# Kernel optimization log

Hardware: AMD Instinct MI355X
Metric: run time of the kernel (lower is better)

The kernel has to match this reference:

```python
import jax, jax.numpy as jnp
import numpy as np

T, B, D = 20, 1024, 2312  # time_steps, batch, 2*34*34 (NMNIST flattened)


def setup_inputs() -> dict:
    key = jax.random.key(0)
    k1, k2, k3, k4 = jax.random.split(key, 4)
    return {
        "x": jax.random.normal(k1, (T, B, D), dtype=jnp.float32),
        # ATIC per-feature parameters (torch inits these to zero; small random
        # values used here so gradients/gating are non-trivial for kernel tests)
        "ac": jax.random.normal(k2, (D,), dtype=jnp.float32) * 0.1,
        "tw": jax.random.normal(k3, (D,), dtype=jnp.float32) * 0.1,
        "ig": jax.random.normal(k4, (D,), dtype=jnp.float32) * 0.1,
        # LIF scalar parameters (torch defaults)
        "membrane_decay": jnp.asarray(0.8, dtype=jnp.float32),
        "synaptic_decay": jnp.asarray(0.75, dtype=jnp.float32),
        "threshold": jnp.asarray(0.8, dtype=jnp.float32),
    }


def _atic(xt, ac, tw, ig):
    # AdaptiveTemporalInformationCompression.forward on one timestep [B, D]
    p = jax.nn.softmax(xt, axis=-1)
    entropy = -jnp.sum(p * jnp.log(p + 1e-8), axis=-1)          # [B]
    compression_mask = jax.nn.sigmoid(ac * entropy[:, None])    # [B, D]
    compressed = xt * compression_mask * jax.nn.sigmoid(tw) * jax.nn.sigmoid(ig)
    binding_strength = jnp.mean(jnp.abs(compressed))             # scalar
    return compressed * binding_strength


def reference(x, ac, tw, ig, membrane_decay, synaptic_decay, threshold):
    # Per-timestep ATIC gating feeding a LIF current/membrane recurrence with
    # sigmoid surrogate spikes (surrogate_alpha = 1.0) and soft reset.
    def step(carry, xt):
        i, v = carry
        i = synaptic_decay * i + _atic(xt, ac, tw, ig)
        v = membrane_decay * v + i
        s = jax.nn.sigmoid(v - threshold)  # surrogate spike
        v = v - s * threshold              # soft reset toward reset_potential=0
        return (i, v), s

    init = (jnp.zeros((B, D), x.dtype), jnp.zeros((B, D), x.dtype))
    _, spikes = jax.lax.scan(step, init, x)  # [T, B, D]
    return spikes
```

## Files before the change

kernel.cpp:

```cpp
#include <hip/hip_runtime.h>

#define T_STEPS 20
#define B_SIZE  1024
#define D_SIZE  2312
#define BD      (B_SIZE * D_SIZE)
#define BLOCK   256
#define ROW_F4  (D_SIZE / 4)
#define ROWS_PER_BLOCK 4

#define ACC_STRIDE 32
#define ENT_OFF    1024
#define GEFF_OFF   (ENT_OFF + T_STEPS * B_SIZE)
#define WS_WORDS   (GEFF_OFF + D_SIZE)

typedef float floatx4 __attribute__((ext_vector_type(4)));

__device__ __forceinline__ float sigmoidf_(float x) {
    return 1.0f / (1.0f + __expf(-x));
}

__device__ __forceinline__ float waveReduceMax(float v) {
    #pragma unroll
    for (int o = 32; o > 0; o >>= 1) v = fmaxf(v, __shfl_xor(v, o, 64));
    return v;
}

__device__ __forceinline__ float waveReduceSum(float v) {
    #pragma unroll
    for (int o = 32; o > 0; o >>= 1) v += __shfl_xor(v, o, 64);
    return v;
}

__device__ __forceinline__ void waveReduceSum2(float& a, float& b) {
    #pragma unroll
    for (int o = 32; o > 0; o >>= 1) {
        a += __shfl_xor(a, o, 64);
        b += __shfl_xor(b, o, 64);
    }
}

__global__ void prep_kernel(const float* __restrict__ tw, const float* __restrict__ ig,
                            float* __restrict__ ws) {
    const int i = blockIdx.x * BLOCK + threadIdx.x;
    if (i < T_STEPS * ACC_STRIDE) ws[i] = 0.0f;
    if (i < D_SIZE) ws[GEFF_OFF + i] = sigmoidf_(tw[i]) * sigmoidf_(ig[i]);
}

__global__ void __launch_bounds__(BLOCK)
phase1_entropy(const float* __restrict__ x, const float* __restrict__ ac,
               float* __restrict__ ws) {
    const int lane = threadIdx.x & 63;
    const int tb   = blockIdx.x * ROWS_PER_BLOCK + (threadIdx.x >> 6);
    const int t    = tb >> 10;
    const bool tail = (lane < (ROW_F4 - 9 * 64));

    const float4* __restrict__ xr = (const float4*)(x + (size_t)tb * D_SIZE);

    float4 xv[10];
    float m_l = -1e30f;
    #pragma unroll
    for (int k = 0; k < 9; ++k) {
        xv[k] = xr[lane + (k << 6)];
        m_l = fmaxf(fmaxf(m_l, fmaxf(xv[k].x, xv[k].y)),
                    fmaxf(xv[k].z, xv[k].w));
    }
    xv[9] = tail ? xr[576 + lane]
                 : make_float4(-1e30f, -1e30f, -1e30f, -1e30f);
    m_l = fmaxf(fmaxf(m_l, fmaxf(xv[9].x, xv[9].y)),
                fmaxf(xv[9].z, xv[9].w));
    const float m = waveReduceMax(m_l);

    float Z = 0.0f, W = 0.0f;
    #pragma unroll
    for (int k = 0; k < 10; ++k) {
        const float u0 = xv[k].x - m, u1 = xv[k].y - m;
        const float u2 = xv[k].z - m, u3 = xv[k].w - m;
        const float e0 = __expf(u0), e1 = __expf(u1);
        const float e2 = __expf(u2), e3 = __expf(u3);
        Z += (e0 + e1) + (e2 + e3);
        W += (e0 * u0 + e1 * u1) + (e2 * u2 + e3 * u3);
    }
    waveReduceSum2(Z, W);
    const float H = __logf(Z) - W / Z;

    const float4* __restrict__ ac4 = (const float4*)ac;
    const float4* __restrict__ g4  = (const float4*)(ws + GEFF_OFF);
    float s_l = 0.0f;
    #pragma unroll
    for (int k = 0; k < 9; ++k) {
        const int f = lane + (k << 6);
        const float4 a = ac4[f];
        const float4 g = g4[f];
        s_l += fabsf(xv[k].x * sigmoidf_(a.x * H) * g.x)
             + fabsf(xv[k].y * sigmoidf_(a.y * H) * g.y)
             + fabsf(xv[k].z * sigmoidf_(a.z * H) * g.z)
             + fabsf(xv[k].w * sigmoidf_(a.w * H) * g.w);
    }
    if (tail) {
        const int f = 576 + lane;
        const float4 a = ac4[f];
        const float4 g = g4[f];
        s_l += fabsf(xv[9].x * sigmoidf_(a.x * H) * g.x)
             + fabsf(xv[9].y * sigmoidf_(a.y * H) * g.y)
             + fabsf(xv[9].z * sigmoidf_(a.z * H) * g.z)
             + fabsf(xv[9].w * sigmoidf_(a.w * H) * g.w);
    }
    s_l = waveReduceSum(s_l);
    if (lane == 0) {
        atomicAdd(&ws[ACC_STRIDE * t], s_l);
        ws[ENT_OFF + tb] = H;
    }
}

__global__ void __launch_bounds__(BLOCK)
phase2_lif(const float* __restrict__ x, const float* __restrict__ ac,
           const float* __restrict__ ws,
           const float* __restrict__ mdp, const float* __restrict__ sdp,
           const float* __restrict__ thp, float* __restrict__ out) {
    const int idx = blockIdx.x * BLOCK + threadIdx.x;
    const int e0  = idx * 4;
    const int b   = e0 / D_SIZE;
    const int d0  = e0 - b * D_SIZE;

    const float md = mdp[0];
    const float sd = sdp[0];
    const float th = thp[0];
    const float invBD = 1.0f / (float)BD;

    const float4 a = *(const float4*)(ac + d0);
    const float4 g = *(const float4*)(ws + GEFF_OFF + d0);

    float i0 = 0.f, i1 = 0.f, i2 = 0.f, i3 = 0.f;
    float v0 = 0.f, v1 = 0.f, v2 = 0.f, v3 = 0.f;

    for (int t = 0; t < T_STEPS; ++t) {
        const float4 xv = *(const float4*)(x + (size_t)t * BD + e0);
        const float H  = ws[ENT_OFF + t * B_SIZE + b];
        const float bs = ws[ACC_STRIDE * t] * invBD;

        const float c0 = xv.x * sigmoidf_(a.x * H) * g.x * bs;
        const float c1 = xv.y * sigmoidf_(a.y * H) * g.y * bs;
        const float c2 = xv.z * sigmoidf_(a.z * H) * g.z * bs;
        const float c3 = xv.w * sigmoidf_(a.w * H) * g.w * bs;

        i0 = sd * i0 + c0;  v0 = md * v0 + i0;
        i1 = sd * i1 + c1;  v1 = md * v1 + i1;
        i2 = sd * i2 + c2;  v2 = md * v2 + i2;
        i3 = sd * i3 + c3;  v3 = md * v3 + i3;

        const float s0 = sigmoidf_(v0 - th);
        const float s1 = sigmoidf_(v1 - th);
        const float s2 = sigmoidf_(v2 - th);
        const float s3 = sigmoidf_(v3 - th);
        v0 -= s0 * th;  v1 -= s1 * th;  v2 -= s2 * th;  v3 -= s3 * th;

        floatx4 sv = { s0, s1, s2, s3 };
        __builtin_nontemporal_store(sv, (floatx4*)(out + (size_t)t * BD + e0));
    }
}

extern "C" void kernel_launch(void* const* d_in, const int* in_sizes, int n_in,
                              void* d_out, int out_size, void* d_ws, size_t ws_size,
                              hipStream_t stream) {
    const float* x   = (const float*)d_in[0];
    const float* ac  = (const float*)d_in[1];
    const float* tw  = (const float*)d_in[2];
    const float* ig  = (const float*)d_in[3];
    const float* mdp = (const float*)d_in[4];
    const float* sdp = (const float*)d_in[5];
    const float* thp = (const float*)d_in[6];
    float* out = (float*)d_out;
    float* ws  = (float*)d_ws;

    prep_kernel<<<10, BLOCK, 0, stream>>>(tw, ig, ws);

    phase1_entropy<<<(T_STEPS * B_SIZE) / ROWS_PER_BLOCK, BLOCK, 0, stream>>>(x, ac, ws);

    phase2_lif<<<BD / 4 / BLOCK, BLOCK, 0, stream>>>(x, ac, ws, mdp, sdp, thp, out);
}
```

Baseline: 381.4 us.

## Remove prep kernel and atomics; use per-block partial sums reduced in phase2

Drops the separate prep kernel. Each phase1 block now recomputes the sigmoid(tw)*sigmoid(ig) gate into shared memory. The global atomicAdd on the per-timestep binding sum is replaced by per-block partial sums written to the workspace, and every phase2 block reduces these into shared memory before its LIF loop. The point is to save one kernel launch and avoid atomic contention on 20 addresses. In exchange, the gate and the partial-sum reduction are recomputed redundantly in every block, and phase1 gains a block-level sync.

Measured after the change: 372.7 us. 2.3% less time.

```diff
diff --git a/kernel.cpp b/kernel.cpp
--- a/kernel.cpp
+++ b/kernel.cpp
@@ -7,11 +7,10 @@
 #define BLOCK   256
 #define ROW_F4  (D_SIZE / 4)
 #define ROWS_PER_BLOCK 4
-
-#define ACC_STRIDE 32
-#define ENT_OFF    1024
-#define GEFF_OFF   (ENT_OFF + T_STEPS * B_SIZE)
-#define WS_WORDS   (GEFF_OFF + D_SIZE)
+#define PART_N  (B_SIZE / ROWS_PER_BLOCK)
+
+#define ENT_OFF (T_STEPS * PART_N)
+#define WS_WORDS (ENT_OFF + T_STEPS * B_SIZE)
 
 typedef float floatx4 __attribute__((ext_vector_type(4)));
 
@@ -19,19 +18,17 @@
     return 1.0f / (1.0f + __expf(-x));
 }
 
-__device__ __forceinline__ float waveReduceMax(float v) {
+__device__ __forceinline__ float wredMax(float v) {
     #pragma unroll
     for (int o = 32; o > 0; o >>= 1) v = fmaxf(v, __shfl_xor(v, o, 64));
     return v;
 }
-
-__device__ __forceinline__ float waveReduceSum(float v) {
+__device__ __forceinline__ float wredSum(float v) {
     #pragma unroll
     for (int o = 32; o > 0; o >>= 1) v += __shfl_xor(v, o, 64);
     return v;
 }
-
-__device__ __forceinline__ void waveReduceSum2(float& a, float& b) {
+__device__ __forceinline__ void wredSum2(float& a, float& b) {
     #pragma unroll
     for (int o = 32; o > 0; o >>= 1) {
         a += __shfl_xor(a, o, 64);
@@ -39,19 +36,35 @@
     }
 }
 
-__global__ void prep_kernel(const float* __restrict__ tw, const float* __restrict__ ig,
-                            float* __restrict__ ws) {
-    const int i = blockIdx.x * BLOCK + threadIdx.x;
-    if (i < T_STEPS * ACC_STRIDE) ws[i] = 0.0f;
-    if (i < D_SIZE) ws[GEFF_OFF + i] = sigmoidf_(tw[i]) * sigmoidf_(ig[i]);
-}
-
 __global__ void __launch_bounds__(BLOCK)
 phase1_entropy(const float* __restrict__ x, const float* __restrict__ ac,
+               const float* __restrict__ tw, const float* __restrict__ ig,
                float* __restrict__ ws) {
-    const int lane = threadIdx.x & 63;
-    const int tb   = blockIdx.x * ROWS_PER_BLOCK + (threadIdx.x >> 6);
-    const int t    = tb >> 10;
+    __shared__ float4 g4s[ROW_F4];
+    __shared__ float  ss[4];
+
+    const int tid  = threadIdx.x;
+    const int lane = tid & 63;
+    const int wid  = tid >> 6;
+
+    const float4* __restrict__ tw4 = (const float4*)tw;
+    const float4* __restrict__ ig4 = (const float4*)ig;
+    #pragma unroll
+    for (int k = 0; k < 3; ++k) {
+        const int f = tid + (k << 8);
+        if (k < 2 || tid < (ROW_F4 - 2 * BLOCK)) {
+            const float4 t4 = tw4[f], i4 = ig4[f];
+            float4 gg;
+            gg.x = sigmoidf_(t4.x) * sigmoidf_(i4.x);
+            gg.y = sigmoidf_(t4.y) * sigmoidf_(i4.y);
+            gg.z = sigmoidf_(t4.z) * sigmoidf_(i4.z);
+            gg.w = sigmoidf_(t4.w) * sigmoidf_(i4.w);
+            g4s[f] = gg;
+        }
+    }
+    __syncthreads();
+
+    const int tb   = (blockIdx.x << 2) | wid;
     const bool tail = (lane < (ROW_F4 - 9 * 64));
 
     const float4* __restrict__ xr = (const float4*)(x + (size_t)tb * D_SIZE);
@@ -68,7 +81,7 @@
                  : make_float4(-1e30f, -1e30f, -1e30f, -1e30f);
     m_l = fmaxf(fmaxf(m_l, fmaxf(xv[9].x, xv[9].y)),
                 fmaxf(xv[9].z, xv[9].w));
-    const float m = waveReduceMax(m_l);
+    const float m = wredMax(m_l);
 
     float Z = 0.0f, W = 0.0f;
     #pragma unroll
@@ -80,17 +93,16 @@
         Z += (e0 + e1) + (e2 + e3);
         W += (e0 * u0 + e1 * u1) + (e2 * u2 + e3 * u3);
     }
-    waveReduceSum2(Z, W);
+    wredSum2(Z, W);
     const float H = __logf(Z) - W / Z;
 
     const float4* __restrict__ ac4 = (const float4*)ac;
-    const float4* __restrict__ g4  = (const float4*)(ws + GEFF_OFF);
     float s_l = 0.0f;
     #pragma unroll
     for (int k = 0; k < 9; ++k) {
         const int f = lane + (k << 6);
         const float4 a = ac4[f];
-        const float4 g = g4[f];
+        const float4 g = g4s[f];
         s_l += fabsf(xv[k].x * sigmoidf_(a.x * H) * g.x)
              + fabsf(xv[k].y * sigmoidf_(a.y * H) * g.y)
              + fabsf(xv[k].z * sigmoidf_(a.z * H) * g.z)
@@ -99,25 +111,47 @@
     if (tail) {
         const int f = 576 + lane;
         const float4 a = ac4[f];
-        const float4 g = g4[f];
+        const float4 g = g4s[f];
         s_l += fabsf(xv[9].x * sigmoidf_(a.x * H) * g.x)
              + fabsf(xv[9].y * sigmoidf_(a.y * H) * g.y)
              + fabsf(xv[9].z * sigmoidf_(a.z * H) * g.z)
              + fabsf(xv[9].w * sigmoidf_(a.w * H) * g.w);
     }
-    s_l = waveReduceSum(s_l);
+    s_l = wredSum(s_l);
     if (lane == 0) {
-        atomicAdd(&ws[ACC_STRIDE * t], s_l);
+        ss[wid] = s_l;
         ws[ENT_OFF + tb] = H;
     }
+    __syncthreads();
+    if (tid == 0)
+        ws[blockIdx.x] = (ss[0] + ss[1]) + (ss[2] + ss[3]);
 }
 
 __global__ void __launch_bounds__(BLOCK)
 phase2_lif(const float* __restrict__ x, const float* __restrict__ ac,
+           const float* __restrict__ tw, const float* __restrict__ ig,
            const float* __restrict__ ws,
            const float* __restrict__ mdp, const float* __restrict__ sdp,
            const float* __restrict__ thp, float* __restrict__ out) {
-    const int idx = blockIdx.x * BLOCK + threadIdx.x;
+    __shared__ float sbs[T_STEPS];
+
+    const int tid  = threadIdx.x;
+    const int lane = tid & 63;
+    const int wid  = tid >> 6;
+    const float invBD = 1.0f / (float)BD;
+
+    #pragma unroll
+    for (int q = 0; q < 5; ++q) {
+        const int t = wid * 5 + q;
+        float a = 0.0f;
+        #pragma unroll
+        for (int j = 0; j < 4; ++j) a += ws[t * PART_N + lane + (j << 6)];
+        a = wredSum(a);
+        if (lane == 0) sbs[t] = a * invBD;
+    }
+    __syncthreads();
+
+    const int idx = blockIdx.x * BLOCK + tid;
     const int e0  = idx * 4;
     const int b   = e0 / D_SIZE;
     const int d0  = e0 - b * D_SIZE;
@@ -125,10 +159,15 @@
     const float md = mdp[0];
     const float sd = sdp[0];
     const float th = thp[0];
-    const float invBD = 1.0f / (float)BD;
-
-    const float4 a = *(const float4*)(ac + d0);
-    const float4 g = *(const float4*)(ws + GEFF_OFF + d0);
+
+    const float4 a  = *(const float4*)(ac + d0);
+    const float4 t4 = *(const float4*)(tw + d0);
+    const float4 i4g = *(const float4*)(ig + d0);
+    float4 g;
+    g.x = sigmoidf_(t4.x) * sigmoidf_(i4g.x);
+    g.y = sigmoidf_(t4.y) * sigmoidf_(i4g.y);
+    g.z = sigmoidf_(t4.z) * sigmoidf_(i4g.z);
+    g.w = sigmoidf_(t4.w) * sigmoidf_(i4g.w);
 
     float i0 = 0.f, i1 = 0.f, i2 = 0.f, i3 = 0.f;
     float v0 = 0.f, v1 = 0.f, v2 = 0.f, v3 = 0.f;
@@ -136,7 +175,7 @@
     for (int t = 0; t < T_STEPS; ++t) {
         const float4 xv = *(const float4*)(x + (size_t)t * BD + e0);
         const float H  = ws[ENT_OFF + t * B_SIZE + b];
-        const float bs = ws[ACC_STRIDE * t] * invBD;
+        const float bs = sbs[t];
 
         const float c0 = xv.x * sigmoidf_(a.x * H) * g.x * bs;
         const float c1 = xv.y * sigmoidf_(a.y * H) * g.y * bs;
@@ -172,9 +211,9 @@
     float* out = (float*)d_out;
     float* ws  = (float*)d_ws;
 
-    prep_kernel<<<10, BLOCK, 0, stream>>>(tw, ig, ws);
-
-    phase1_entropy<<<(T_STEPS * B_SIZE) / ROWS_PER_BLOCK, BLOCK, 0, stream>>>(x, ac, ws);
-
-    phase2_lif<<<BD / 4 / BLOCK, BLOCK, 0, stream>>>(x, ac, ws, mdp, sdp, thp, out);
-}
+    phase1_entropy<<<(T_STEPS * B_SIZE) / ROWS_PER_BLOCK, BLOCK, 0, stream>>>(
+        x, ac, tw, ig, ws);
+
+    phase2_lif<<<BD / 4 / BLOCK, BLOCK, 0, stream>>>(
+        x, ac, tw, ig, ws, mdp, sdp, thp, out);
+}
```
